# Kernel tuning notes

Measured on AMD Instinct MI355X. Metric: run time of the kernel, lower is better.

Reference implementation:

```python
import jax, jax.numpy as jnp
import numpy as np

B, S, E, H = 2, 2048, 1024, 16
D = E // H  # head_dim = 64


def setup_inputs() -> dict:
    key = jax.random.key(0)
    ks = jax.random.split(key, 4)
    return {
        "hidden_states": jax.random.normal(ks[0], (B, S, E), jnp.float32),
        "qk_weight": jax.random.normal(ks[1], (E, 2 * E), jnp.float32) * 0.02,
        "qk_bias": jnp.zeros((2 * E,), jnp.float32),
        "v_weight": jax.random.normal(ks[2], (E, E), jnp.float32) * 0.02,
        "v_resid_gain": jnp.ones((), jnp.float32),
        "v_skip_gain": jnp.ones((), jnp.float32),
        "proj_weight": jax.random.normal(ks[3], (E, E), jnp.float32) * 0.02,
        "proj_resid_gain": jnp.ones((), jnp.float32),
        "proj_skip_gain": jnp.ones((), jnp.float32),
        "attn_mat_resid_gain": jnp.ones((H,), jnp.float32),
        "attn_mat_skip_gain": jnp.ones((H,), jnp.float32),
        "centre_attn_gain": jnp.ones((H,), jnp.float32),
    }


def reference(hidden_states, qk_weight, qk_bias, v_weight, v_resid_gain,
              v_skip_gain, proj_weight, proj_resid_gain, proj_skip_gain,
              attn_mat_resid_gain, attn_mat_skip_gain, centre_attn_gain):
    b, s, e = hidden_states.shape
    dt = hidden_states.dtype
    eye_e = jnp.eye(e, dtype=dt)

    # qk_attn: MyConv1D (standard linear), split into query/key
    qk = hidden_states @ qk_weight + qk_bias
    q, k = jnp.split(qk, 2, axis=-1)
    # v_attn: skip MyConv1D -> x @ (resid_gain * W + skip_gain * I), no bias
    v = hidden_states @ (v_resid_gain * v_weight + v_skip_gain * eye_e)

    def split_heads(t):  # [b,s,e] -> [b,h,s,d]
        return t.reshape(b, s, H, D).transpose(0, 2, 1, 3)

    q, k, v = split_heads(q), split_heads(k), split_heads(v)

    # scaled causal attention scores
    scores = jnp.einsum('bhqd,bhkd->bhqk', q, k) / jnp.asarray(D, dt) ** 0.5
    causal = jnp.tril(jnp.ones((s, s), bool))
    scores = jnp.where(causal, scores, jnp.finfo(dt).min)
    attn = jax.nn.softmax(scores, axis=-1)

    # shaped attention: gain-mix softmax probs with identity and causal-uniform
    uniform = jnp.tril(jnp.ones((s, s), dt) / jnp.arange(1, s + 1, dtype=dt)[:, None])
    g_r = attn_mat_resid_gain[None, :, None, None]
    g_s = attn_mat_skip_gain[None, :, None, None]
    g_c = centre_attn_gain[None, :, None, None]
    new_attn = g_r * attn + g_s * jnp.eye(s, dtype=dt) - g_c * uniform

    ctx = jnp.einsum('bhqk,bhkd->bhqd', new_attn, v)
    ctx = ctx.transpose(0, 2, 1, 3).reshape(b, s, e)  # merge heads
    # c_proj: skip MyConv1D, no bias
    out = ctx @ (proj_resid_gain * proj_weight + proj_skip_gain * eye_e)
    return out
```

## Files before the change

kernel.cpp:

```cpp
#include <hip/hip_runtime.h>

typedef __bf16 bf16;
typedef __attribute__((ext_vector_type(8))) __bf16 bf16x8;
typedef __attribute__((ext_vector_type(4))) float f32x4;

union U16x8 { uint4 u; bf16 h[8]; };
union Pack4 { uint2 u2; bf16 h[4]; };

#define QSCALE 0.18033688011112042f

__device__ __forceinline__ void async16(const bf16* g, bf16* l) {
    __builtin_amdgcn_global_load_lds((const __attribute__((address_space(1))) void*)g,
                                     (__attribute__((address_space(3))) void*)l, 16, 0, 0);
}

__device__ const int QT_OF[40] = {15,15,15,15,14,14,14,14,13,13,13,13,12,12,12,12,
                                  11,11,11,10,10,10,9,9,9,8,8,8,7,7,6,6,5,5,4,4,3,2,1,0};
__device__ const int CK_OF[40] = {0,1,2,3,0,1,2,3,0,1,2,3,0,1,2,3,
                                  0,1,2,0,1,2,0,1,2,0,1,2,0,1,0,1,0,1,0,1,0,0,0,0};
__device__ const int BASE_OF[16] = {39,38,37,36,34,32,30,28,25,22,19,16,12,8,4,0};

__global__ void prep(const float* __restrict__ hs, bf16* __restrict__ hsb,
                     const float* __restrict__ qkw, const float* __restrict__ vw,
                     const float* __restrict__ pw, bf16* __restrict__ qkvT,
                     bf16* __restrict__ pwT, float* __restrict__ csum,
                     const float* __restrict__ vrg, const float* __restrict__ vsg,
                     const float* __restrict__ prg, const float* __restrict__ psg) {
    const int K = 1024;
    int bx = blockIdx.x;
    if (bx < 8) {
        float4* p = (float4*)csum + (bx * 256 + threadIdx.x) * 16;
        #pragma unroll
        for (int i = 0; i < 16; i++) p[i] = make_float4(0.f, 0.f, 0.f, 0.f);
        return;
    }
    if (bx < 4104) {
        int i = ((bx - 8) * 256 + threadIdx.x) * 4;
        float4 f = *(const float4*)(hs + i);
        hsb[i + 0] = (bf16)f.x; hsb[i + 1] = (bf16)f.y;
        hsb[i + 2] = (bf16)f.z; hsb[i + 3] = (bf16)f.w;
        return;
    }
    int r = bx - 4104;
    int z = r < 2048 ? 0 : (r < 3072 ? 1 : 2);
    int q = z == 0 ? r : (z == 1 ? r - 2048 : r - 3072);
    int ntiles = z == 0 ? 64 : 32;
    int N = z == 0 ? 2048 : 1024;
    const float* W = z == 0 ? qkw : (z == 1 ? vw : pw);
    bf16* WT = z == 0 ? qkvT : (z == 1 ? qkvT + (size_t)2 * 1024 * 1024 : pwT);
    float g0 = z == 0 ? 1.f : (z == 1 ? vrg[0] : prg[0]);
    float g1 = z == 0 ? 0.f : (z == 1 ? vsg[0] : psg[0]);

    __shared__ float tile[32][33];
    int n0 = (q % ntiles) * 32, k0 = (q / ntiles) * 32;
    int tx = threadIdx.x & 31, ty = threadIdx.x >> 5;
    #pragma unroll
    for (int rr = 0; rr < 32; rr += 8)
        tile[ty + rr][tx] = W[(size_t)(k0 + ty + rr) * N + n0 + tx];
    __syncthreads();
    #pragma unroll
    for (int rr = 0; rr < 32; rr += 8) {
        int n = n0 + ty + rr, k = k0 + tx;
        float v = g0 * tile[tx][ty + rr] + ((n == k) ? g1 : 0.f);
        if (z == 0 && n < 1024) v *= QSCALE;
        WT[(size_t)n * K + k] = (bf16)v;
    }
}

template<int BN>
__global__ __launch_bounds__(256, 3)
void gemm_bt(const bf16* __restrict__ A, const bf16* __restrict__ BT,
             int M, int N, int K, void* __restrict__ Cout,
             bf16* __restrict__ C2T, float* __restrict__ csum,
             int mode, const float* __restrict__ aux) {
    __shared__ __align__(16) bf16 As[128][64];
    __shared__ __align__(16) bf16 Bs[BN][64];
    constexpr int JF = BN / 32;
    int bid = blockIdx.x;
    int g32 = bid & 31;
    int m0 = ((g32 & 7) * 4 + (g32 >> 3)) * 128;
    int n0 = (bid >> 5) * BN;
    int t = threadIdx.x, lane = t & 63, w = t >> 6;
    int wm = (w >> 1) * 64, wn = (w & 1) * (BN / 2);
    int lrow = lane & 15, lkg = lane >> 4;

    f32x4 acc[4][JF] = {};

    int gsw = ((lane & 7) ^ ((lane >> 3) & 7)) * 8;
    const bf16* Ab = A + (size_t)(m0 + w * 8 + (lane >> 3)) * K + gsw;
    const bf16* Bb = BT + (size_t)(n0 + w * 8 + (lane >> 3)) * K + gsw;

    for (int k0 = 0; k0 < K; k0 += 64) {
        #pragma unroll
        for (int p = 0; p < 4; p++)
            async16(Ab + (size_t)(p * 32) * K + k0, &As[p * 32 + w * 8][0]);
        #pragma unroll
        for (int p = 0; p < BN / 32; p++)
            async16(Bb + (size_t)(p * 32) * K + k0, &Bs[p * 32 + w * 8][0]);
        __syncthreads();
        #pragma unroll
        for (int ks = 0; ks < 2; ks++) {
            bf16x8 af[4], bfr[JF];
            int phys = (((4 * ks + lkg) ^ (lrow & 7)) << 3);
            #pragma unroll
            for (int i = 0; i < 4; i++) af[i] = *(const bf16x8*)&As[wm + i * 16 + lrow][phys];
            #pragma unroll
            for (int j = 0; j < JF; j++) bfr[j] = *(const bf16x8*)&Bs[wn + j * 16 + lrow][phys];
            #pragma unroll
            for (int i = 0; i < 4; i++)
                #pragma unroll
                for (int j = 0; j < JF; j++)
                    acc[i][j] = __builtin_amdgcn_mfma_f32_16x16x32_bf16(af[i], bfr[j], acc[i][j], 0, 0, 0);
        }
        __syncthreads();
    }

    int rgrp = (lane >> 4) * 4;
    #pragma unroll
    for (int i = 0; i < 4; i++) {
        #pragma unroll
        for (int j = 0; j < JF; j++) {
            int col = n0 + wn + j * 16 + lrow;
            int row0 = m0 + wm + i * 16 + rgrp;
            if (mode == 0) {
                if (col < 2048) {
                    float bb = aux[col];
                    if (col < 1024) bb *= QSCALE;
                    #pragma unroll
                    for (int reg = 0; reg < 4; reg++)
                        ((bf16*)Cout)[(size_t)(row0 + reg) * 2048 + col] = (bf16)(acc[i][j][reg] + bb);
                } else {
                    int c = col - 2048;
                    Pack4 p4;
                    #pragma unroll
                    for (int reg = 0; reg < 4; reg++) p4.h[reg] = (bf16)acc[i][j][reg];
                    *(uint2*)&C2T[(size_t)c * 4096 + row0] = p4.u2;
                }
            } else {
                #pragma unroll
                for (int reg = 0; reg < 4; reg++)
                    ((float*)Cout)[(size_t)(row0 + reg) * N + col] = acc[i][j][reg];
            }
        }
    }

    if (mode == 0 && n0 >= 2048) {
        int chunkb = (m0 + wm) >> 5;
        #pragma unroll
        for (int j = 0; j < JF; j++) {
            float s0 = 0.f, s1 = 0.f;
            #pragma unroll
            for (int reg = 0; reg < 4; reg++) {
                s0 += acc[0][j][reg] + acc[1][j][reg];
                s1 += acc[2][j][reg] + acc[3][j][reg];
            }
            s0 += __shfl_xor(s0, 16, 64); s0 += __shfl_xor(s0, 32, 64);
            s1 += __shfl_xor(s1, 16, 64); s1 += __shfl_xor(s1, 32, 64);
            if (lkg == 0) {
                int col = n0 - 2048 + wn + j * 16 + lrow;
                atomicAdd(&csum[(size_t)col * 128 + chunkb], s0);
                atomicAdd(&csum[(size_t)col * 128 + chunkb + 1], s1);
            }
        }
    }
}

__global__ __launch_bounds__(256, 3)
void flash_split(const bf16* __restrict__ qk, const bf16* __restrict__ vT,
                 bf16* __restrict__ Opart, float* __restrict__ lbuf,
                 int S, int E, int H) {
    __shared__ __align__(16) bf16 Ks[2][64][64];
    __shared__ __align__(16) bf16 Vt[2][64][64];
    __shared__ __align__(16) bf16 Ps[4][32][72];

    int item = blockIdx.x, bh = blockIdx.y;
    int qt = QT_OF[item], ck = CK_OF[item];
    int b = bh >> 4, h = bh & 15;
    int q0 = qt * 128;
    int ktstart = ck * 8;
    int nloc = min(8, 2 * (qt + 1) - ktstart);
    int t = threadIdx.x, lane = t & 63, w = t >> 6;
    int lrow = lane & 15, lkg = lane >> 4;
    const int ld = 2 * E;

    const bf16* Qg  = qk + (size_t)(b * S + q0) * ld + h * 64;
    const bf16* Kg0 = qk + (size_t)(b * S) * ld + E + h * 64;
    const bf16* Vg0 = vT + (size_t)(h * 64) * 4096 + b * 2048;

    bf16x8 qf[2][2];
    #pragma unroll
    for (int qg = 0; qg < 2; qg++)
        #pragma unroll
        for (int ks = 0; ks < 2; ks++)
            qf[qg][ks] = *(const bf16x8*)&Qg[(size_t)(32 * w + 16 * qg + lrow) * ld + ks * 32 + lkg * 8];

    f32x4 oacc[4][2] = {};
    float lrun[2] = {0.f, 0.f};

    auto stage = [&](int buf, int kt) {
        int k0 = kt * 64;
        int g = (lane & 7) ^ ((lane >> 3) & 7);
        #pragma unroll
        for (int p = 0; p < 2; p++) {
            int row = w * 8 + p * 32 + (lane >> 3);
            async16(Kg0 + (size_t)(k0 + row) * ld + g * 8, &Ks[buf][row][(lane & 7) * 8]);
            async16(Vg0 + (size_t)row * 4096 + k0 + g * 8, &Vt[buf][row][(lane & 7) * 8]);
        }
    };

    stage(0, ktstart);
    for (int kl = 0; kl < nloc; kl++) {
        int buf = kl & 1;
        int k0 = (ktstart + kl) * 64;
        __syncthreads();
        if (kl + 1 < nloc) stage(1 - buf, ktstart + kl + 1);

        bool skip0 = (k0 > q0 + 32 * w + 15);
        bool skip1 = (k0 > q0 + 32 * w + 31);
        if (skip0 && skip1) continue;

        f32x4 sacc[2][4] = {};
        #pragma unroll
        for (int ks = 0; ks < 2; ks++) {
            bf16x8 ak[4];
            int phys = (((4 * ks + lkg) ^ (lrow & 7)) << 3);
            #pragma unroll
            for (int kf = 0; kf < 4; kf++)
                ak[kf] = *(const bf16x8*)&Ks[buf][16 * kf + lrow][phys];
            #pragma unroll
            for (int kf = 0; kf < 4; kf++)
                sacc[0][kf] = __builtin_amdgcn_mfma_f32_16x16x32_bf16(ak[kf], qf[0][ks], sacc[0][kf], 0, 0, 0);
            if (!skip1)
                #pragma unroll
                for (int kf = 0; kf < 4; kf++)
                    sacc[1][kf] = __builtin_amdgcn_mfma_f32_16x16x32_bf16(ak[kf], qf[1][ks], sacc[1][kf], 0, 0, 0);
        }

        #pragma unroll
        for (int qg = 0; qg < 2; qg++) {
            if ((qg == 0 && skip0) || (qg == 1 && skip1)) continue;
            int kmin = q0 + 32 * w + 16 * qg;
            float rsum = 0.f;
            if (k0 + 63 <= kmin) {
                #pragma unroll
                for (int kf = 0; kf < 4; kf++) {
                    Pack4 p4;
                    #pragma unroll
                    for (int r = 0; r < 4; r++) {
                        float p = exp2f(sacc[qg][kf][r]);
                        rsum += p;
                        p4.h[r] = (bf16)p;
                    }
                    *(uint2*)&Ps[w][16 * qg + lrow][16 * kf + 4 * lkg] = p4.u2;
                }
            } else {
                int qrow = kmin + lrow;
                #pragma unroll
                for (int kf = 0; kf < 4; kf++) {
                    Pack4 p4;
                    #pragma unroll
                    for (int r = 0; r < 4; r++) {
                        float sv = sacc[qg][kf][r];
                        if (k0 + 16 * kf + 4 * lkg + r > qrow) sv = -1e30f;
                        float p = exp2f(sv);
                        rsum += p;
                        p4.h[r] = (bf16)p;
                    }
                    *(uint2*)&Ps[w][16 * qg + lrow][16 * kf + 4 * lkg] = p4.u2;
                }
            }
            lrun[qg] += rsum;
        }

        #pragma unroll
        for (int ks = 0; ks < 2; ks++) {
            bf16x8 av[4];
            int phys = (((4 * ks + lkg) ^ (lrow & 7)) << 3);
            #pragma unroll
            for (int df = 0; df < 4; df++)
                av[df] = *(const bf16x8*)&Vt[buf][16 * df + lrow][phys];
            #pragma unroll
            for (int qg = 0; qg < 2; qg++) {
                if ((qg == 0 && skip0) || (qg == 1 && skip1)) continue;
                bf16x8 bp = *(const bf16x8*)&Ps[w][16 * qg + lrow][ks * 32 + lkg * 8];
                #pragma unroll
                for (int df = 0; df < 4; df++)
                    oacc[df][qg] = __builtin_amdgcn_mfma_f32_16x16x32_bf16(av[df], bp, oacc[df][qg], 0, 0, 0);
            }
        }
    }

    size_t ibase = (size_t)(bh * 40 + item) * 128;
    #pragma unroll
    for (int qg = 0; qg < 2; qg++) {
        #pragma unroll
        for (int df = 0; df < 4; df++) {
            Pack4 p4;
            #pragma unroll
            for (int r = 0; r < 4; r++) p4.h[r] = (bf16)oacc[df][qg][r];
            *(uint2*)&Ps[w][16 * qg + lrow][16 * df + 4 * lkg] = p4.u2;
        }
        float l = lrun[qg];
        l += __shfl_xor(l, 16, 64);
        l += __shfl_xor(l, 32, 64);
        if (lkg == 0) lbuf[ibase + w * 32 + qg * 16 + lrow] = l;
    }
    int r_l = lane >> 1, half = lane & 1;
    bf16* orow = Opart + (ibase + w * 32 + r_l) * 64 + 32 * half;
    #pragma unroll
    for (int c = 0; c < 4; c++)
        *(uint4*)&orow[8 * c] = *(const uint4*)&Ps[w][r_l][32 * half + 8 * c];
}

__global__ void merge_combine(const bf16* __restrict__ Opart, const float* __restrict__ lbuf,
                              const bf16* __restrict__ vT, const float* __restrict__ csum,
                              const float* __restrict__ gr, const float* __restrict__ gs,
                              const float* __restrict__ gc, bf16* __restrict__ ctx) {
    const int S = 2048, E = 1024;
    int qt = blockIdx.x, bh = blockIdx.y;
    int b = bh >> 4, h = bh & 15;
    int nc = (qt >> 2) + 1, base = BASE_OF[qt];
    int q0 = qt * 128;
    int t = threadIdx.x;

    __shared__ bf16 osm[128][66];

    {
        int r = t >> 1, dh = (t & 1) * 32;
        float L = 0.f;
        for (int c = 0; c < nc; c++)
            L += lbuf[(size_t)(bh * 40 + base + c) * 128 + r];
        float inv = 1.f / L;
        float o[32] = {};
        for (int c = 0; c < nc; c++) {
            const bf16* src = Opart + ((size_t)(bh * 40 + base + c) * 128 + r) * 64 + dh;
            #pragma unroll
            for (int g = 0; g < 4; g++) {
                U16x8 u; u.u = *(const uint4*)&src[g * 8];
                #pragma unroll
                for (int j = 0; j < 8; j++) o[g * 8 + j] += (float)u.h[j];
            }
        }
        #pragma unroll
        for (int j = 0; j < 32; j++) osm[r][dh + j] = (bf16)(o[j] * inv);
    }
    __syncthreads();

    {
        int c = t & 63, sc = t >> 6;
        int col = h * 64 + c;
        int row0 = q0 + sc * 32;
        float grh = gr[h], gsh = gs[h], gch = gc[h];
        int cend = qt * 4 + sc;
        const float4* cs4 = (const float4*)(csum + (size_t)col * 128 + b * 64);
        float run = 0.f;
        #pragma unroll
        for (int g = 0; g < 16; g++) {
            float4 f = cs4[g];
            int j = g * 4;
            run += (j + 0 < cend ? f.x : 0.f) + (j + 1 < cend ? f.y : 0.f)
                 + (j + 2 < cend ? f.z : 0.f) + (j + 3 < cend ? f.w : 0.f);
        }
        const bf16* vrow = vT + (size_t)col * 4096 + b * 2048 + row0;
        U16x8 vv[4];
        #pragma unroll
        for (int g = 0; g < 4; g++) vv[g].u = *(const uint4*)&vrow[g * 8];
        bf16* cp = ctx + ((size_t)(b * S + row0)) * E + col;
        #pragma unroll
        for (int i = 0; i < 32; i++) {
            float v = (float)vv[i >> 3].h[i & 7];
            run += v;
            float pm = run / (float)(row0 + i + 1);
            cp[(size_t)i * E] = (bf16)(grh * (float)osm[sc * 32 + i][c] + gsh * v - gch * pm);
        }
    }
}

extern "C" void kernel_launch(void* const* d_in, const int* in_sizes, int n_in,
                              void* d_out, int out_size, void* d_ws, size_t ws_size,
                              hipStream_t stream) {
    const float* hs  = (const float*)d_in[0];
    const float* qkw = (const float*)d_in[1];
    const float* qkb = (const float*)d_in[2];
    const float* vw  = (const float*)d_in[3];
    const float* vrg = (const float*)d_in[4];
    const float* vsg = (const float*)d_in[5];
    const float* pw  = (const float*)d_in[6];
    const float* prg = (const float*)d_in[7];
    const float* psg = (const float*)d_in[8];
    const float* amr = (const float*)d_in[9];
    const float* ams = (const float*)d_in[10];
    const float* amc = (const float*)d_in[11];
    float* out = (float*)d_out;

    const int B = 2, S = 2048, E = 1024, H = 16, M = B * S;
    char* ws = (char*)d_ws;
    size_t off = 0;
    auto alloc = [&](size_t bytes) { void* p = ws + off; off += (bytes + 255) & ~255ull; return p; };
    bf16* hsb   = (bf16*)alloc((size_t)M * E * 2);
    bf16* qkvT  = (bf16*)alloc((size_t)3 * E * E * 2);
    bf16* pwT   = (bf16*)alloc((size_t)E * E * 2);
    bf16* qko   = (bf16*)alloc((size_t)M * 2 * E * 2);
    bf16* vT    = (bf16*)alloc((size_t)E * M * 2);
    float* csum = (float*)alloc((size_t)E * 128 * 4);
    bf16* ctxb  = (bf16*)alloc((size_t)M * E * 2);
    bf16* Opart = (bf16*)alloc((size_t)32 * 40 * 128 * 64 * 2);
    float* lbuf = (float*)alloc((size_t)32 * 40 * 128 * 4);

    prep<<<8200, 256, 0, stream>>>(hs, hsb, qkw, vw, pw, qkvT, pwT, csum, vrg, vsg, prg, psg);

    gemm_bt<128><<<32 * (3 * E / 128), 256, 0, stream>>>(
        hsb, qkvT, M, 3 * E, E, qko, vT, csum, 0, qkb);

    flash_split<<<dim3(40, 32), 256, 0, stream>>>(qko, vT, Opart, lbuf, S, E, H);
    merge_combine<<<dim3(16, 32), 256, 0, stream>>>(Opart, lbuf, vT, csum, amr, ams, amc, ctxb);

    gemm_bt<64><<<32 * (E / 64), 256, 0, stream>>>(
        ctxb, pwT, M, E, E, out, nullptr, nullptr, 2, nullptr);
}
```

Before: 205.1 us.

## Keep softmax probabilities in registers by permuting V staging layout

The P matrix no longer round-trips through a per-wave LDS buffer. The exp2 outputs are packed directly into MFMA B-operand registers, and V is staged with 4-byte async loads into a permuted column order so that the key index ordering matches the register layout of the S accumulator. Dropping the Ps buffer shrinks LDS to 32KB and allows the launch bound to raise occupancy to 4 blocks. The cost is four times as many smaller global-to-LDS transactions for V, plus an extra barrier before the epilogue reuses smem.

```diff
diff --git a/kernel.cpp b/kernel.cpp
--- a/kernel.cpp
+++ b/kernel.cpp
@@ -12,6 +12,10 @@
 __device__ __forceinline__ void async16(const bf16* g, bf16* l) {
     __builtin_amdgcn_global_load_lds((const __attribute__((address_space(1))) void*)g,
                                      (__attribute__((address_space(3))) void*)l, 16, 0, 0);
+}
+__device__ __forceinline__ void async4(const bf16* g, bf16* l) {
+    __builtin_amdgcn_global_load_lds((const __attribute__((address_space(1))) void*)g,
+                                     (__attribute__((address_space(3))) void*)l, 4, 0, 0);
 }
 
 __device__ const int QT_OF[40] = {15,15,15,15,14,14,14,14,13,13,13,13,12,12,12,12,
@@ -165,13 +169,13 @@
     }
 }
 
-__global__ __launch_bounds__(256, 3)
+__global__ __launch_bounds__(256, 4)
 void flash_split(const bf16* __restrict__ qk, const bf16* __restrict__ vT,
                  bf16* __restrict__ Opart, float* __restrict__ lbuf,
                  int S, int E, int H) {
-    __shared__ __align__(16) bf16 Ks[2][64][64];
-    __shared__ __align__(16) bf16 Vt[2][64][64];
-    __shared__ __align__(16) bf16 Ps[4][32][72];
+    __shared__ __align__(16) bf16 smem[16384];
+    #define KS(bu, r, c) smem[(bu) * 4096 + (r) * 64 + (c)]
+    #define VT(bu, r, c) smem[8192 + (bu) * 4096 + (r) * 64 + (c)]
 
     int item = blockIdx.x, bh = blockIdx.y;
     int qt = QT_OF[item], ck = CK_OF[item];
@@ -203,8 +207,16 @@
         #pragma unroll
         for (int p = 0; p < 2; p++) {
             int row = w * 8 + p * 32 + (lane >> 3);
-            async16(Kg0 + (size_t)(k0 + row) * ld + g * 8, &Ks[buf][row][(lane & 7) * 8]);
-            async16(Vg0 + (size_t)row * 4096 + k0 + g * 8, &Vt[buf][row][(lane & 7) * 8]);
+            async16(Kg0 + (size_t)(k0 + row) * ld + g * 8, &KS(buf, row, (lane & 7) * 8));
+        }
+        int gcol = lane & 31;
+        #pragma unroll
+        for (int it = 0; it < 8; it++) {
+            int row = it * 8 + w * 2 + (lane >> 5);
+            int lb = (gcol >> 2) ^ (row & 7);
+            int kk = ((lb >> 2) << 5) | (((gcol >> 1) & 1) << 4)
+                   | ((lb & 3) << 2) | ((gcol & 1) << 1);
+            async4(Vg0 + (size_t)row * 4096 + k0 + kk, &VT(buf, row, gcol * 2));
         }
     };
 
@@ -226,7 +238,7 @@
             int phys = (((4 * ks + lkg) ^ (lrow & 7)) << 3);
             #pragma unroll
             for (int kf = 0; kf < 4; kf++)
-                ak[kf] = *(const bf16x8*)&Ks[buf][16 * kf + lrow][phys];
+                ak[kf] = *(const bf16x8*)&KS(buf, 16 * kf + lrow, phys);
             #pragma unroll
             for (int kf = 0; kf < 4; kf++)
                 sacc[0][kf] = __builtin_amdgcn_mfma_f32_16x16x32_bf16(ak[kf], qf[0][ks], sacc[0][kf], 0, 0, 0);
@@ -236,6 +248,7 @@
                     sacc[1][kf] = __builtin_amdgcn_mfma_f32_16x16x32_bf16(ak[kf], qf[1][ks], sacc[1][kf], 0, 0, 0);
         }
 
+        bf16x8 bp[2][2];
         #pragma unroll
         for (int qg = 0; qg < 2; qg++) {
             if ((qg == 0 && skip0) || (qg == 1 && skip1)) continue;
@@ -243,31 +256,25 @@
             float rsum = 0.f;
             if (k0 + 63 <= kmin) {
                 #pragma unroll
-                for (int kf = 0; kf < 4; kf++) {
-                    Pack4 p4;
+                for (int kf = 0; kf < 4; kf++)
                     #pragma unroll
                     for (int r = 0; r < 4; r++) {
                         float p = exp2f(sacc[qg][kf][r]);
                         rsum += p;
-                        p4.h[r] = (bf16)p;
+                        bp[qg][kf >> 1][(kf & 1) * 4 + r] = (bf16)p;
                     }
-                    *(uint2*)&Ps[w][16 * qg + lrow][16 * kf + 4 * lkg] = p4.u2;
-                }
             } else {
                 int qrow = kmin + lrow;
                 #pragma unroll
-                for (int kf = 0; kf < 4; kf++) {
-                    Pack4 p4;
+                for (int kf = 0; kf < 4; kf++)
                     #pragma unroll
                     for (int r = 0; r < 4; r++) {
                         float sv = sacc[qg][kf][r];
                         if (k0 + 16 * kf + 4 * lkg + r > qrow) sv = -1e30f;
                         float p = exp2f(sv);
                         rsum += p;
-                        p4.h[r] = (bf16)p;
+                        bp[qg][kf >> 1][(kf & 1) * 4 + r] = (bf16)p;
                     }
-                    *(uint2*)&Ps[w][16 * qg + lrow][16 * kf + 4 * lkg] = p4.u2;
-                }
             }
             lrun[qg] += rsum;
         }
@@ -278,18 +285,19 @@
             int phys = (((4 * ks + lkg) ^ (lrow & 7)) << 3);
             #pragma unroll
             for (int df = 0; df < 4; df++)
-                av[df] = *(const bf16x8*)&Vt[buf][16 * df + lrow][phys];
+                av[df] = *(const bf16x8*)&VT(buf, 16 * df + lrow, phys);
             #pragma unroll
             for (int qg = 0; qg < 2; qg++) {
                 if ((qg == 0 && skip0) || (qg == 1 && skip1)) continue;
-                bf16x8 bp = *(const bf16x8*)&Ps[w][16 * qg + lrow][ks * 32 + lkg * 8];
                 #pragma unroll
                 for (int df = 0; df < 4; df++)
-                    oacc[df][qg] = __builtin_amdgcn_mfma_f32_16x16x32_bf16(av[df], bp, oacc[df][qg], 0, 0, 0);
-            }
-        }
-    }
-
+                    oacc[df][qg] = __builtin_amdgcn_mfma_f32_16x16x32_bf16(av[df], bp[qg][ks], oacc[df][qg], 0, 0, 0);
+            }
+        }
+    }
+
+    __syncthreads();
+    bf16* eps = smem;
     size_t ibase = (size_t)(bh * 40 + item) * 128;
     #pragma unroll
     for (int qg = 0; qg < 2; qg++) {
@@ -298,7 +306,7 @@
             Pack4 p4;
             #pragma unroll
             for (int r = 0; r < 4; r++) p4.h[r] = (bf16)oacc[df][qg][r];
-            *(uint2*)&Ps[w][16 * qg + lrow][16 * df + 4 * lkg] = p4.u2;
+            *(uint2*)&eps[(size_t)(w * 32 + 16 * qg + lrow) * 72 + 16 * df + 4 * lkg] = p4.u2;
         }
         float l = lrun[qg];
         l += __shfl_xor(l, 16, 64);
@@ -309,7 +317,9 @@
     bf16* orow = Opart + (ibase + w * 32 + r_l) * 64 + 32 * half;
     #pragma unroll
     for (int c = 0; c < 4; c++)
-        *(uint4*)&orow[8 * c] = *(const uint4*)&Ps[w][r_l][32 * half + 8 * c];
+        *(uint4*)&orow[8 * c] = *(const uint4*)&eps[(size_t)(w * 32 + r_l) * 72 + 32 * half + 8 * c];
+    #undef KS
+    #undef VT
 }
 
 __global__ void merge_combine(const bf16* __restrict__ Opart, const float* __restrict__ lbuf,
```

Result: slower. 272.2 us (+32.7%).
